# Kernel optimization log

Measured on AMD Instinct MI355X. Metric: run time of the kernel, lower is better.

## Reference

```python
import jax, jax.numpy as jnp
import numpy as np
import math

V, D, L, H, F, S_MAX = 32000, 512, 4, 8, 2048, 1024
DK = D // H
EPS = 1e-6


def _ln(x, g, b):
    # torch: gamma*(x-mean)/(std+eps)+beta with unbiased=False std, eps added to std
    mean = jnp.mean(x, axis=-1, keepdims=True)
    std = jnp.sqrt(jnp.mean((x - mean) ** 2, axis=-1, keepdims=True))
    return g * (x - mean) / (std + EPS) + b


def _pos_encoding(seq_len, d_model):
    pos = jnp.arange(seq_len, dtype=jnp.float32)[:, None]
    div = jnp.exp(jnp.arange(0, d_model, 2, dtype=jnp.float32) * (-math.log(10000.0) / d_model))
    pe = jnp.zeros((seq_len, d_model), dtype=jnp.float32)
    pe = pe.at[:, 0::2].set(jnp.sin(pos * div))
    pe = pe.at[:, 1::2].set(jnp.cos(pos * div))
    return pe


def setup_inputs() -> dict:
    key = jax.random.key(0)
    ks = jax.random.split(key, 20)
    n = lambda k, shape, s=0.02: (jax.random.normal(k, shape, dtype=jnp.float32) * s)
    inp = {
        "input_tokens": jax.random.randint(ks[0], (4, 1024), 0, V, dtype=jnp.int64),
        "tok_emb": n(ks[1], (V, D)),
        "gamma1": jnp.ones((L, D), jnp.float32), "beta1": jnp.zeros((L, D), jnp.float32),
        "wq": n(ks[2], (L, D, D)), "bq": jnp.zeros((L, D), jnp.float32),
        "wk": n(ks[3], (L, D, D)), "bk": jnp.zeros((L, D), jnp.float32),
        "wv": n(ks[4], (L, D, D)), "bv": jnp.zeros((L, D), jnp.float32),
        "wo": n(ks[5], (L, D, D)), "bo": jnp.zeros((L, D), jnp.float32),
        "gamma2": jnp.ones((L, D), jnp.float32), "beta2": jnp.zeros((L, D), jnp.float32),
        "w1": n(ks[6], (L, D, F)), "b1": jnp.zeros((L, F), jnp.float32),
        "w2": n(ks[7], (L, F, D)), "b2": jnp.zeros((L, D), jnp.float32),
        "gamma_f": jnp.ones((D,), jnp.float32), "beta_f": jnp.zeros((D,), jnp.float32),
        "w_out": n(ks[8], (D, V)), "b_out": jnp.zeros((V,), jnp.float32),
    }
    return inp


def reference(input_tokens, tok_emb, gamma1, beta1, wq, bq, wk, bk, wv, bv, wo, bo,
              gamma2, beta2, w1, b1, w2, b2, gamma_f, beta_f, w_out, b_out):
    B, S = input_tokens.shape
    # embedding * sqrt(d_model) + sinusoidal PE (dropout = identity in eval)
    x = tok_emb[input_tokens] * jnp.float32(math.sqrt(D)) + _pos_encoding(S, D)[None]
    causal = jnp.tril(jnp.ones((S, S), dtype=bool))[None, None]  # [1,1,S,S]
    scale = jnp.float32(1.0 / math.sqrt(DK))

    def block(x, p):
        g1, be1, Wq, Bq, Wk, Bk, Wv, Bv, Wo, Bo, g2, be2, W1, B1, W2, B2 = p
        h = _ln(x, g1, be1)
        q = (h @ Wq + Bq).reshape(B, S, H, DK).transpose(0, 2, 1, 3)
        k = (h @ Wk + Bk).reshape(B, S, H, DK).transpose(0, 2, 1, 3)
        v = (h @ Wv + Bv).reshape(B, S, H, DK).transpose(0, 2, 1, 3)
        scores = jnp.einsum('bhqd,bhkd->bhqk', q, k) * scale
        scores = jnp.where(causal, scores, jnp.float32(-1e9))  # masked_fill
        attn = jax.nn.softmax(scores, axis=-1)
        o = jnp.einsum('bhqk,bhkd->bhqd', attn, v)
        o = o.transpose(0, 2, 1, 3).reshape(B, S, D) @ Wo + Bo
        x = x + o
        h2 = _ln(x, g2, be2)
        ff = jax.nn.gelu(h2 @ W1 + B1, approximate=False) @ W2 + B2
        return x + ff, None

    params = (gamma1, beta1, wq, bq, wk, bk, wv, bv, wo, bo, gamma2, beta2, w1, b1, w2, b2)
    x, _ = jax.lax.scan(block, x, params)
    x = _ln(x, gamma_f, beta_f)
    logits = x @ w_out + b_out
    return logits
```

## Files before the change

kernel.cpp:

```cpp
#include <hip/hip_runtime.h>
#include <cstdint>
#include <cstddef>

typedef __attribute__((ext_vector_type(8))) short short8;
typedef __attribute__((ext_vector_type(4))) float f32x4;

#define DEV static __device__ __forceinline__

DEV short f2bf(float f) {
  unsigned u = __float_as_uint(f);
  u = (u + 0x7fffu + ((u >> 16) & 1u)) >> 16;
  return (short)u;
}

DEV void gload_lds16(const void* g, void* l) {
  __builtin_amdgcn_global_load_lds(
      (const __attribute__((address_space(1))) unsigned int*)(uintptr_t)g,
      (__attribute__((address_space(3))) unsigned int*)(uintptr_t)l,
      16, 0, 0);
}

DEV size_t swz_src(int c, int K, int k0) {
  int r = c >> 2;
  return (size_t)r * K + k0 + (size_t)(((c ^ r) & 3) << 3);
}

DEV void transpose_tile32(const float* __restrict__ src, int sld,
                          short* __restrict__ dst, int dld,
                          int sr, int sc, int tid)
{
  __shared__ float tile[32][33];
  const int r = tid >> 5, c = tid & 31;
#pragma unroll
  for (int i = 0; i < 4; ++i)
    tile[r + 8 * i][c] = src[(size_t)(sr + r + 8 * i) * sld + sc + c];
  __syncthreads();
#pragma unroll
  for (int i = 0; i < 4; ++i)
    dst[(size_t)(sc + r + 8 * i) * dld + sr + c] = f2bf(tile[c][r + 8 * i]);
}

__global__ __launch_bounds__(256) void convert_all_k(
    const float* __restrict__ wq, const float* __restrict__ wk,
    const float* __restrict__ wv, const float* __restrict__ wo,
    const float* __restrict__ w1, const float* __restrict__ w2,
    const float* __restrict__ wout,
    const float* __restrict__ bq, const float* __restrict__ bk,
    const float* __restrict__ bv,
    short* __restrict__ wqkv_bt, short* __restrict__ wo_bt,
    short* __restrict__ w1_bt, short* __restrict__ w2_bt,
    short* __restrict__ wout_bt, float* __restrict__ bqkv)
{
  const int t = blockIdx.x, tid = threadIdx.x;
  if (t < 3072) {
    int layer = t / 768, rem = t % 768, mat = rem / 256, tt = rem % 256;
    int tr = tt / 16, tc = tt % 16;
    const float* src = (mat == 0 ? wq : mat == 1 ? wk : wv) + (size_t)layer * 262144;
    short* dst = wqkv_bt + (size_t)layer * 786432 + (size_t)mat * 262144;
    transpose_tile32(src, 512, dst, 512, tr * 32, tc * 32, tid);
  } else if (t < 4096) {
    int t2 = t - 3072;
    int layer = t2 / 256, tt = t2 % 256, tr = tt / 16, tc = tt % 16;
    transpose_tile32(wo + (size_t)layer * 262144, 512,
                     wo_bt + (size_t)layer * 262144, 512, tr * 32, tc * 32, tid);
  } else if (t < 8192) {
    int t2 = t - 4096;
    int layer = t2 / 1024, tt = t2 % 1024, tr = tt / 64, tc = tt % 64;
    transpose_tile32(w1 + (size_t)layer * 1048576, 2048,
                     w1_bt + (size_t)layer * 1048576, 512, tr * 32, tc * 32, tid);
  } else if (t < 12288) {
    int t2 = t - 8192;
    int layer = t2 / 1024, tt = t2 % 1024, tr = tt / 16, tc = tt % 16;
    transpose_tile32(w2 + (size_t)layer * 1048576, 512,
                     w2_bt + (size_t)layer * 1048576, 2048, tr * 32, tc * 32, tid);
  } else if (t < 28288) {
    int t2 = t - 12288;
    int tr = t2 / 1000, tc = t2 % 1000;
    transpose_tile32(wout, 32000, wout_bt, 512, tr * 32, tc * 32, tid);
  } else {
    int idx = (t - 28288) * 256 + tid;
    int layer = idx / 1536, j = idx % 1536;
    float v = (j < 512) ? bq[layer * 512 + j]
            : (j < 1024) ? bk[layer * 512 + j - 512]
                         : bv[layer * 512 + j - 1024];
    bqkv[idx] = v;
  }
}

__global__ __launch_bounds__(256) void embed_k(
    const int* __restrict__ tok, const float* __restrict__ emb, float* __restrict__ x)
{
  int idx = blockIdx.x * 256 + threadIdx.x;
  int d = idx & 511, bs = idx >> 9, s = bs & 1023;
  int t = tok[bs];
  float dv = expf((float)(d & ~1) * (-9.210340371976184f / 512.f));
  float ang = (float)s * dv;
  float pe = (d & 1) ? cosf(ang) : sinf(ang);
  x[idx] = emb[(size_t)t * 512 + d] * 22.62741699796952f + pe;
}

__global__ __launch_bounds__(256) void layernorm_k(
    const float* __restrict__ x, const float* __restrict__ g,
    const float* __restrict__ b, short* __restrict__ out)
{
  const int row = blockIdx.x, tid = threadIdx.x;
  const float* xr = x + (size_t)row * 512;
  float v0 = xr[tid], v1 = xr[tid + 256];
  float s = v0 + v1;
  __shared__ float rs[4], rq[4];
#pragma unroll
  for (int o = 32; o > 0; o >>= 1) s += __shfl_down(s, o, 64);
  if ((tid & 63) == 0) rs[tid >> 6] = s;
  __syncthreads();
  float mean = (rs[0] + rs[1] + rs[2] + rs[3]) * (1.f / 512.f);
  float d0 = v0 - mean, d1 = v1 - mean;
  float q = d0 * d0 + d1 * d1;
#pragma unroll
  for (int o = 32; o > 0; o >>= 1) q += __shfl_down(q, o, 64);
  if ((tid & 63) == 0) rq[tid >> 6] = q;
  __syncthreads();
  float var = (rq[0] + rq[1] + rq[2] + rq[3]) * (1.f / 512.f);
  float inv = 1.f / (sqrtf(var) + 1e-6f);
  out[(size_t)row * 512 + tid]       = f2bf(g[tid] * d0 * inv + b[tid]);
  out[(size_t)row * 512 + tid + 256] = f2bf(g[tid + 256] * d1 * inv + b[tid + 256]);
}

template<bool GELU, bool RES, bool OUTBF16>
__global__ __launch_bounds__(256) void gemm_bt(
    const short* __restrict__ A, const short* __restrict__ Bt,
    const float* __restrict__ bias, const float* __restrict__ resid,
    void* __restrict__ out, int M, int N, int K)
{
  __shared__ __align__(16) short lA[128 * 32];
  __shared__ __align__(16) short lB[128 * 32];
  const int tid = threadIdx.x;
  const int lane = tid & 63;
  const int w = tid >> 6, wr = w >> 1, wc = w & 1;
  const int lr = lane & 15, quad = lane >> 4;
  const int m0 = blockIdx.y * 128, n0 = blockIdx.x * 128;

  f32x4 acc[4][4] = {};

  const int c1 = tid, c2 = tid + 256;
  const short* Ab = A + (size_t)m0 * K;
  const short* Bb = Bt + (size_t)n0 * K;
  const int sl = ((quad ^ lr) & 3) << 3;

  for (int k0 = 0; k0 < K; k0 += 32) {
    gload_lds16(Ab + swz_src(c1, K, k0), lA + c1 * 8);
    gload_lds16(Ab + swz_src(c2, K, k0), lA + c2 * 8);
    gload_lds16(Bb + swz_src(c1, K, k0), lB + c1 * 8);
    gload_lds16(Bb + swz_src(c2, K, k0), lB + c2 * 8);
    __syncthreads();
    short8 af[4], bf[4];
#pragma unroll
    for (int mi = 0; mi < 4; ++mi)
      af[mi] = *(const short8*)&lA[(wr * 64 + mi * 16 + lr) * 32 + sl];
#pragma unroll
    for (int ni = 0; ni < 4; ++ni)
      bf[ni] = *(const short8*)&lB[(wc * 64 + ni * 16 + lr) * 32 + sl];
#pragma unroll
    for (int mi = 0; mi < 4; ++mi)
#pragma unroll
      for (int ni = 0; ni < 4; ++ni)
        acc[mi][ni] = __builtin_amdgcn_mfma_f32_16x16x32_bf16(af[mi], bf[ni], acc[mi][ni], 0, 0, 0);
    __syncthreads();
  }

#pragma unroll
  for (int mi = 0; mi < 4; ++mi) {
#pragma unroll
    for (int ni = 0; ni < 4; ++ni) {
      const int n = n0 + wc * 64 + ni * 16 + lr;
      const float bn = bias[n];
#pragma unroll
      for (int r = 0; r < 4; ++r) {
        const int m = m0 + wr * 64 + mi * 16 + quad * 4 + r;
        float v = acc[mi][ni][r] + bn;
        if (GELU) v = 0.5f * v * (1.f + erff(v * 0.7071067811865475f));
        if (RES) v += resid[(size_t)m * N + n];
        if (OUTBF16) ((short*)out)[(size_t)m * N + n] = f2bf(v);
        else         ((float*)out)[(size_t)m * N + n] = v;
      }
    }
  }
}

template<bool GELU, bool RES, bool OUTBF16>
__global__ __launch_bounds__(256) void gemm64_bt(
    const short* __restrict__ A, const short* __restrict__ Bt,
    const float* __restrict__ bias, const float* __restrict__ resid,
    void* __restrict__ out, int M, int N, int K)
{
  __shared__ __align__(16) short lA[64 * 32];
  __shared__ __align__(16) short lB[128 * 32];
  const int tid = threadIdx.x;
  const int lane = tid & 63;
  const int w = tid >> 6;
  const int lr = lane & 15, quad = lane >> 4;
  const int m0 = blockIdx.y * 64, n0 = blockIdx.x * 128;

  f32x4 acc[4][2] = {};

  const int c2 = tid + 256;
  const short* Ab = A + (size_t)m0 * K;
  const short* Bb = Bt + (size_t)n0 * K;
  const int sl = ((quad ^ lr) & 3) << 3;

  for (int k0 = 0; k0 < K; k0 += 32) {
    gload_lds16(Ab + swz_src(tid, K, k0), lA + tid * 8);
    gload_lds16(Bb + swz_src(tid, K, k0), lB + tid * 8);
    gload_lds16(Bb + swz_src(c2,  K, k0), lB + c2 * 8);
    __syncthreads();
    short8 af[4], bf[2];
#pragma unroll
    for (int mi = 0; mi < 4; ++mi)
      af[mi] = *(const short8*)&lA[(mi * 16 + lr) * 32 + sl];
#pragma unroll
    for (int ni = 0; ni < 2; ++ni)
      bf[ni] = *(const short8*)&lB[(w * 32 + ni * 16 + lr) * 32 + sl];
#pragma unroll
    for (int mi = 0; mi < 4; ++mi)
#pragma unroll
      for (int ni = 0; ni < 2; ++ni)
        acc[mi][ni] = __builtin_amdgcn_mfma_f32_16x16x32_bf16(af[mi], bf[ni], acc[mi][ni], 0, 0, 0);
    __syncthreads();
  }

#pragma unroll
  for (int mi = 0; mi < 4; ++mi) {
#pragma unroll
    for (int ni = 0; ni < 2; ++ni) {
      const int n = n0 + w * 32 + ni * 16 + lr;
      const float bn = bias[n];
#pragma unroll
      for (int r = 0; r < 4; ++r) {
        const int m = m0 + mi * 16 + quad * 4 + r;
        float v = acc[mi][ni][r] + bn;
        if (GELU) v = 0.5f * v * (1.f + erff(v * 0.7071067811865475f));
        if (RES) v += resid[(size_t)m * N + n];
        if (OUTBF16) ((short*)out)[(size_t)m * N + n] = f2bf(v);
        else         ((float*)out)[(size_t)m * N + n] = v;
      }
    }
  }
}

__global__ __launch_bounds__(256) void attn_k(
    const short* __restrict__ qkv, short* __restrict__ attn_out)
{
  const int bh = blockIdx.y, b = bh >> 3, h = bh & 7;
  const int q0 = blockIdx.x * 64;
  const int tid = threadIdx.x, lane = tid & 63, w = tid >> 6;
  const int lr = lane & 15, quad = lane >> 4;
  const int RS = 1536;

  const short* qb = qkv + (size_t)b * 1024 * RS + h * 64;
  const short* kb = qb + 512;
  const short* vb = qb + 1024;

  __shared__ __align__(16) short lK[32 * 64];
  __shared__ __align__(16) short lVt[64 * 32];
  __shared__ __align__(16) short lP[4][16 * 32];

  const int qrow = q0 + w * 16 + lr;
  const short8 aq0 = *(const short8*)(qb + (size_t)qrow * RS + quad * 8);
  const short8 aq1 = *(const short8*)(qb + (size_t)qrow * RS + 32 + quad * 8);

  f32x4 o[4] = {};
  float mrow[4] = {-1e30f, -1e30f, -1e30f, -1e30f};
  float lrow[4] = {0.f, 0.f, 0.f, 0.f};

  const int kend = q0 + 64;
  for (int kt = 0; kt < kend; kt += 32) {
    {
      int r = tid >> 3, c = (tid & 7) * 8;
      gload_lds16(kb + (size_t)(kt + r) * RS + c, lK + r * 64 + c);
      short8 vv = *(const short8*)(vb + (size_t)(kt + r) * RS + c);
#pragma unroll
      for (int j = 0; j < 8; ++j) lVt[(c + j) * 32 + r] = vv[j];
    }
    __syncthreads();

    f32x4 st[2];
#pragma unroll
    for (int t = 0; t < 2; ++t) {
      const short8 bk0 = *(const short8*)&lK[(t * 16 + lr) * 64 + quad * 8];
      const short8 bk1 = *(const short8*)&lK[(t * 16 + lr) * 64 + 32 + quad * 8];
      f32x4 z = {0.f, 0.f, 0.f, 0.f};
      z = __builtin_amdgcn_mfma_f32_16x16x32_bf16(aq0, bk0, z, 0, 0, 0);
      z = __builtin_amdgcn_mfma_f32_16x16x32_bf16(aq1, bk1, z, 0, 0, 0);
      st[t] = z;
    }
    float sc[2][4];
#pragma unroll
    for (int t = 0; t < 2; ++t)
#pragma unroll
      for (int r = 0; r < 4; ++r) {
        int qg = q0 + w * 16 + quad * 4 + r;
        int kg = kt + t * 16 + lr;
        sc[t][r] = (kg <= qg) ? st[t][r] * 0.125f : -1e30f;
      }
#pragma unroll
    for (int r = 0; r < 4; ++r) {
      float tm = fmaxf(sc[0][r], sc[1][r]);
#pragma unroll
      for (int off = 1; off < 16; off <<= 1) tm = fmaxf(tm, __shfl_xor(tm, off, 64));
      float mnew = fmaxf(mrow[r], tm);
      float alpha = __expf(mrow[r] - mnew);
      mrow[r] = mnew;
      float p0 = __expf(sc[0][r] - mnew);
      float p1 = __expf(sc[1][r] - mnew);
      lP[w][(quad * 4 + r) * 32 + lr]      = f2bf(p0);
      lP[w][(quad * 4 + r) * 32 + 16 + lr] = f2bf(p1);
      float ps = p0 + p1;
#pragma unroll
      for (int off = 1; off < 16; off <<= 1) ps += __shfl_xor(ps, off, 64);
      lrow[r] = lrow[r] * alpha + ps;
#pragma unroll
      for (int ni = 0; ni < 4; ++ni) o[ni][r] *= alpha;
    }
    const short8 pa = *(const short8*)&lP[w][lr * 32 + quad * 8];
#pragma unroll
    for (int ni = 0; ni < 4; ++ni) {
      const short8 bv = *(const short8*)&lVt[(ni * 16 + lr) * 32 + quad * 8];
      o[ni] = __builtin_amdgcn_mfma_f32_16x16x32_bf16(pa, bv, o[ni], 0, 0, 0);
    }
    __syncthreads();
  }

#pragma unroll
  for (int ni = 0; ni < 4; ++ni)
#pragma unroll
    for (int r = 0; r < 4; ++r) {
      int qg = q0 + w * 16 + quad * 4 + r;
      float val = o[ni][r] / lrow[r];
      attn_out[((size_t)(b * 1024 + qg)) * 512 + h * 64 + ni * 16 + lr] = f2bf(val);
    }
}

extern "C" void kernel_launch(void* const* d_in, const int* in_sizes, int n_in,
                              void* d_out, int out_size, void* d_ws, size_t ws_size,
                              hipStream_t stream)
{
  (void)in_sizes; (void)n_in; (void)out_size; (void)ws_size;
  const int*   tokens  = (const int*)d_in[0];
  const float* tok_emb = (const float*)d_in[1];
  const float* gamma1  = (const float*)d_in[2];
  const float* beta1   = (const float*)d_in[3];
  const float* wq = (const float*)d_in[4];
  const float* bq = (const float*)d_in[5];
  const float* wk = (const float*)d_in[6];
  const float* bk = (const float*)d_in[7];
  const float* wv = (const float*)d_in[8];
  const float* bv = (const float*)d_in[9];
  const float* wo = (const float*)d_in[10];
  const float* bo = (const float*)d_in[11];
  const float* gamma2 = (const float*)d_in[12];
  const float* beta2  = (const float*)d_in[13];
  const float* w1 = (const float*)d_in[14];
  const float* b1 = (const float*)d_in[15];
  const float* w2 = (const float*)d_in[16];
  const float* b2 = (const float*)d_in[17];
  const float* gamma_f = (const float*)d_in[18];
  const float* beta_f  = (const float*)d_in[19];
  const float* w_out   = (const float*)d_in[20];
  const float* b_out   = (const float*)d_in[21];

  char* ws = (char*)d_ws;
  size_t off = 0;
  auto alloc = [&](size_t bytes) -> void* {
    void* p = ws + off; off += (bytes + 255) & ~(size_t)255; return p;
  };
  short* wqkv_bt = (short*)alloc(4ull * 1536 * 512 * 2);
  short* wo_bt   = (short*)alloc(4ull * 512 * 512 * 2);
  short* w1_bt   = (short*)alloc(4ull * 2048 * 512 * 2);
  short* w2_bt   = (short*)alloc(4ull * 512 * 2048 * 2);
  short* wout_bt = (short*)alloc(32000ull * 512 * 2);
  float* bqkv    = (float*)alloc(4ull * 1536 * 4);
  float* x       = (float*)alloc(4096ull * 512 * 4);
  short* hbuf    = (short*)alloc(4096ull * 512 * 2);
  short* qkv     = (short*)alloc(4096ull * 1536 * 2);
  short* attnout = (short*)alloc(4096ull * 512 * 2);
  short* ffn1    = (short*)alloc(4096ull * 2048 * 2);
  short* xf      = (short*)alloc(4096ull * 512 * 2);

  convert_all_k<<<28312, 256, 0, stream>>>(wq, wk, wv, wo, w1, w2, w_out, bq, bk, bv,
                                           wqkv_bt, wo_bt, w1_bt, w2_bt, wout_bt, bqkv);
  embed_k<<<8192, 256, 0, stream>>>(tokens, tok_emb, x);
  for (int l = 0; l < 4; ++l) {
    layernorm_k<<<4096, 256, 0, stream>>>(x, gamma1 + l * 512, beta1 + l * 512, hbuf);
    gemm_bt<false, false, true><<<dim3(12, 32), 256, 0, stream>>>(
        hbuf, wqkv_bt + (size_t)l * 786432, bqkv + l * 1536, nullptr, qkv, 4096, 1536, 512);
    attn_k<<<dim3(16, 32), 256, 0, stream>>>(qkv, attnout);
    gemm64_bt<false, true, false><<<dim3(4, 64), 256, 0, stream>>>(
        attnout, wo_bt + (size_t)l * 262144, bo + l * 512, x, x, 4096, 512, 512);
    layernorm_k<<<4096, 256, 0, stream>>>(x, gamma2 + l * 512, beta2 + l * 512, hbuf);
    gemm_bt<true, false, true><<<dim3(16, 32), 256, 0, stream>>>(
        hbuf, w1_bt + (size_t)l * 1048576, b1 + l * 2048, nullptr, ffn1, 4096, 2048, 512);
    gemm64_bt<false, true, false><<<dim3(4, 64), 256, 0, stream>>>(
        ffn1, w2_bt + (size_t)l * 1048576, b2 + l * 512, x, x, 4096, 512, 2048);
  }
  layernorm_k<<<4096, 256, 0, stream>>>(x, gamma_f, beta_f, xf);
  gemm_bt<false, false, false><<<dim3(250, 32), 256, 0, stream>>>(
      xf, wout_bt, b_out, nullptr, d_out, 4096, 32000, 512);
}
```

Measured before the change: 1.504 ms.

## Double-buffer LDS tiles in GEMM kernels and use 64-row tiles for QKV

Both GEMM kernels now keep two LDS buffers and prefetch the next K-slice with direct global-to-LDS loads while MFMAs run on the current slice, with one barrier per iteration instead of two. The goal is to hide global load latency behind the matrix math. The QKV projection also moves to the 64-row tile kernel so it launches twice as many blocks and fills more CUs. The cost is doubled shared memory per block, which may lower occupancy. The single remaining barrier guards against overwriting a buffer still being read, but nothing explicitly waits for the async prefetch to finish before the data is used.

New measurement: 1.455 ms. 3.2% less time.

```diff
diff --git a/kernel.cpp b/kernel.cpp
--- a/kernel.cpp
+++ b/kernel.cpp
@@ -20,9 +20,9 @@
       16, 0, 0);
 }
 
-DEV size_t swz_src(int c, int K, int k0) {
+DEV size_t swz_src(int c, int K) {
   int r = c >> 2;
-  return (size_t)r * K + k0 + (size_t)(((c ^ r) & 3) << 3);
+  return (size_t)r * K + (size_t)(((c ^ r) & 3) << 3);
 }
 
 DEV void transpose_tile32(const float* __restrict__ src, int sld,
@@ -131,8 +131,8 @@
     const float* __restrict__ bias, const float* __restrict__ resid,
     void* __restrict__ out, int M, int N, int K)
 {
-  __shared__ __align__(16) short lA[128 * 32];
-  __shared__ __align__(16) short lB[128 * 32];
+  __shared__ __align__(16) short lA[2][128 * 32];
+  __shared__ __align__(16) short lB[2][128 * 32];
   const int tid = threadIdx.x;
   const int lane = tid & 63;
   const int w = tid >> 6, wr = w >> 1, wc = w & 1;
@@ -144,27 +144,37 @@
   const int c1 = tid, c2 = tid + 256;
   const short* Ab = A + (size_t)m0 * K;
   const short* Bb = Bt + (size_t)n0 * K;
+  const size_t oa1 = swz_src(c1, K), oa2 = swz_src(c2, K);
   const int sl = ((quad ^ lr) & 3) << 3;
 
+  gload_lds16(Ab + oa1, lA[0] + c1 * 8);
+  gload_lds16(Ab + oa2, lA[0] + c2 * 8);
+  gload_lds16(Bb + oa1, lB[0] + c1 * 8);
+  gload_lds16(Bb + oa2, lB[0] + c2 * 8);
+  __syncthreads();
+
+  int cur = 0;
   for (int k0 = 0; k0 < K; k0 += 32) {
-    gload_lds16(Ab + swz_src(c1, K, k0), lA + c1 * 8);
-    gload_lds16(Ab + swz_src(c2, K, k0), lA + c2 * 8);
-    gload_lds16(Bb + swz_src(c1, K, k0), lB + c1 * 8);
-    gload_lds16(Bb + swz_src(c2, K, k0), lB + c2 * 8);
-    __syncthreads();
+    if (k0 + 32 < K) {
+      gload_lds16(Ab + oa1 + k0 + 32, lA[cur ^ 1] + c1 * 8);
+      gload_lds16(Ab + oa2 + k0 + 32, lA[cur ^ 1] + c2 * 8);
+      gload_lds16(Bb + oa1 + k0 + 32, lB[cur ^ 1] + c1 * 8);
+      gload_lds16(Bb + oa2 + k0 + 32, lB[cur ^ 1] + c2 * 8);
+    }
     short8 af[4], bf[4];
 #pragma unroll
     for (int mi = 0; mi < 4; ++mi)
-      af[mi] = *(const short8*)&lA[(wr * 64 + mi * 16 + lr) * 32 + sl];
+      af[mi] = *(const short8*)&lA[cur][(wr * 64 + mi * 16 + lr) * 32 + sl];
 #pragma unroll
     for (int ni = 0; ni < 4; ++ni)
-      bf[ni] = *(const short8*)&lB[(wc * 64 + ni * 16 + lr) * 32 + sl];
+      bf[ni] = *(const short8*)&lB[cur][(wc * 64 + ni * 16 + lr) * 32 + sl];
 #pragma unroll
     for (int mi = 0; mi < 4; ++mi)
 #pragma unroll
       for (int ni = 0; ni < 4; ++ni)
         acc[mi][ni] = __builtin_amdgcn_mfma_f32_16x16x32_bf16(af[mi], bf[ni], acc[mi][ni], 0, 0, 0);
     __syncthreads();
+    cur ^= 1;
   }
 
 #pragma unroll
@@ -192,8 +202,8 @@
     const float* __restrict__ bias, const float* __restrict__ resid,
     void* __restrict__ out, int M, int N, int K)
 {
-  __shared__ __align__(16) short lA[64 * 32];
-  __shared__ __align__(16) short lB[128 * 32];
+  __shared__ __align__(16) short lA[2][64 * 32];
+  __shared__ __align__(16) short lB[2][128 * 32];
   const int tid = threadIdx.x;
   const int lane = tid & 63;
   const int w = tid >> 6;
@@ -205,26 +215,35 @@
   const int c2 = tid + 256;
   const short* Ab = A + (size_t)m0 * K;
   const short* Bb = Bt + (size_t)n0 * K;
+  const size_t oa1 = swz_src(tid, K), oa2 = swz_src(c2, K);
   const int sl = ((quad ^ lr) & 3) << 3;
 
+  gload_lds16(Ab + oa1, lA[0] + tid * 8);
+  gload_lds16(Bb + oa1, lB[0] + tid * 8);
+  gload_lds16(Bb + oa2, lB[0] + c2 * 8);
+  __syncthreads();
+
+  int cur = 0;
   for (int k0 = 0; k0 < K; k0 += 32) {
-    gload_lds16(Ab + swz_src(tid, K, k0), lA + tid * 8);
-    gload_lds16(Bb + swz_src(tid, K, k0), lB + tid * 8);
-    gload_lds16(Bb + swz_src(c2,  K, k0), lB + c2 * 8);
-    __syncthreads();
+    if (k0 + 32 < K) {
+      gload_lds16(Ab + oa1 + k0 + 32, lA[cur ^ 1] + tid * 8);
+      gload_lds16(Bb + oa1 + k0 + 32, lB[cur ^ 1] + tid * 8);
+      gload_lds16(Bb + oa2 + k0 + 32, lB[cur ^ 1] + c2 * 8);
+    }
     short8 af[4], bf[2];
 #pragma unroll
     for (int mi = 0; mi < 4; ++mi)
-      af[mi] = *(const short8*)&lA[(mi * 16 + lr) * 32 + sl];
+      af[mi] = *(const short8*)&lA[cur][(mi * 16 + lr) * 32 + sl];
 #pragma unroll
     for (int ni = 0; ni < 2; ++ni)
-      bf[ni] = *(const short8*)&lB[(w * 32 + ni * 16 + lr) * 32 + sl];
+      bf[ni] = *(const short8*)&lB[cur][(w * 32 + ni * 16 + lr) * 32 + sl];
 #pragma unroll
     for (int mi = 0; mi < 4; ++mi)
 #pragma unroll
       for (int ni = 0; ni < 2; ++ni)
         acc[mi][ni] = __builtin_amdgcn_mfma_f32_16x16x32_bf16(af[mi], bf[ni], acc[mi][ni], 0, 0, 0);
     __syncthreads();
+    cur ^= 1;
   }
 
 #pragma unroll
@@ -390,7 +409,7 @@
   embed_k<<<8192, 256, 0, stream>>>(tokens, tok_emb, x);
   for (int l = 0; l < 4; ++l) {
     layernorm_k<<<4096, 256, 0, stream>>>(x, gamma1 + l * 512, beta1 + l * 512, hbuf);
-    gemm_bt<false, false, true><<<dim3(12, 32), 256, 0, stream>>>(
+    gemm64_bt<false, false, true><<<dim3(12, 64), 256, 0, stream>>>(
         hbuf, wqkv_bt + (size_t)l * 786432, bqkv + l * 1536, nullptr, qkv, 4096, 1536, 512);
     attn_k<<<dim3(16, 32), 256, 0, stream>>>(qkv, attnout);
     gemm64_bt<false, true, false><<<dim3(4, 64), 256, 0, stream>>>(
```
